# Kernel tuning notes

Hardware: AMD Instinct MI355X
Metric: run time of the kernel (lower is better)

The kernel has to match this reference:

```python
import jax, jax.numpy as jnp
import numpy as np


def _max_pairwise_dist(l, r):
    # l: [N, d], r: [M, d]
    # squared distances via Gram trick: ||l||^2 + ||r||^2 - 2 l.r  -> [N, M]
    l_sq = jnp.sum(l * l, axis=-1)  # [N]
    r_sq = jnp.sum(r * r, axis=-1)  # [M]
    cross = jnp.einsum('nd,md->nm', l, r)  # [N, M]
    sq_dists = l_sq[:, None] + r_sq[None, :] - 2.0 * cross
    sq_dists = jnp.maximum(sq_dists, 0.0)  # guard tiny negatives
    return jnp.sqrt(jnp.max(sq_dists))  # sqrt of max == max of sqrt (monotone)


def setup_inputs() -> dict:
    key = jax.random.key(0)
    k1, k2 = jax.random.split(key)
    N, M, D = 8192, 8192, 64
    return {
        'l_dfa_embeddings': jax.random.normal(k1, (N, D), dtype=jnp.float32),
        'r_dfa_embeddings': jax.random.normal(k2, (M, D), dtype=jnp.float32),
    }


def reference(l_dfa_embeddings, r_dfa_embeddings):
    # Max over all pairwise L2 distances between l and r state embeddings
    return _max_pairwise_dist(l_dfa_embeddings, r_dfa_embeddings)
```

## Files before the change

kernel.cpp:

```cpp
#include <hip/hip_runtime.h>
#include <hip/hip_bf16.h>
#include <math.h>


typedef __attribute__((ext_vector_type(8)))  short  short8;
typedef __attribute__((ext_vector_type(4)))  float  f32x4;
typedef __attribute__((ext_vector_type(16))) float  f32x16;

constexpr int D  = 64;
constexpr int NR = 8192;
constexpr int GX = 32;
constexpr int GY = 64;
constexpr int NSLOT = GX * GY;

__device__ __forceinline__ short f2bf(float f) {
    __hip_bfloat16 h = __float2bfloat16(f);
    return __builtin_bit_cast(short, h);
}


__global__ __launch_bounds__(256) void prepack_kernel(
    const float* __restrict__ L, const float* __restrict__ R,
    short* __restrict__ Apk, short* __restrict__ Bpk,
    float* __restrict__ lsq, float* __restrict__ rsq)
{
    const int t = blockIdx.x * 256 + threadIdx.x;
    const int r = t >> 3;
    const int j = t & 7;
    const int kk = j >> 1, kh = j & 1;
    const bool isL = (r < NR);
    const int rr = isL ? r : r - NR;

    const float* src = (isL ? L : R) + (size_t)rr * D + j * 8;
    short* pk = isL ? Apk : Bpk;

    f32x4 v0 = *reinterpret_cast<const f32x4*>(src + 0);
    f32x4 v1 = *reinterpret_cast<const f32x4*>(src + 4);

    float p = 0.f;
    #pragma unroll
    for (int e = 0; e < 4; ++e) { p = fmaf(v0[e], v0[e], p); p = fmaf(v1[e], v1[e], p); }

    short8 w;
    #pragma unroll
    for (int e = 0; e < 4; ++e) { w[e] = f2bf(v0[e]); w[4+e] = f2bf(v1[e]); }
    *reinterpret_cast<short8*>(
        pk + ((size_t)(rr >> 5) * 4 + kk) * 512 + (kh * 32 + (rr & 31)) * 8) = w;

    p += __shfl_xor(p, 1, 64);
    p += __shfl_xor(p, 2, 64);
    p += __shfl_xor(p, 4, 64);
    if (j == 0) (isL ? lsq : rsq)[rr] = p;
}

__global__ __launch_bounds__(256, 2) void pairdist_mfma_kernel(
    const short* __restrict__ Apk, const short* __restrict__ Bpk,
    const float* __restrict__ lsq, const float* __restrict__ rsq,
    float* __restrict__ slots)
{
    __shared__ __align__(16) short A_lds[4][4][64][8];
    __shared__ __align__(16) short B_lds[4][4][64][8];
    __shared__ __align__(16) float lsq_s[128];
    __shared__ __align__(16) float rsq_s[256];
    __shared__ float wmax_s[4];

    const int tid  = threadIdx.x;
    const int lane = tid & 63;
    const int wave = tid >> 6;
    const int yb = blockIdx.x;
    const int xc = blockIdx.y;

    {
        const short* At = Apk + (size_t)(xc * 4) * 2048;
        #pragma unroll
        for (int i = 0; i < 4; ++i)
            __builtin_amdgcn_global_load_lds(
                (const __attribute__((address_space(1))) unsigned int*)
                    (At + ((size_t)i * 4 + wave) * 512 + lane * 8),
                (__attribute__((address_space(3))) unsigned int*)
                    (&A_lds[i][wave][0][0]),
                16, 0, 0);
    }
    {
        #pragma unroll
        for (int s = 0; s < 4; ++s) {
            const int gsrc = yb * 8 + (s >> 1) * 4 + 2 + (s & 1);
            __builtin_amdgcn_global_load_lds(
                (const __attribute__((address_space(1))) unsigned int*)
                    (Bpk + ((size_t)gsrc * 4 + wave) * 512 + lane * 8),
                (__attribute__((address_space(3))) unsigned int*)
                    (&B_lds[s][wave][0][0]),
                16, 0, 0);
        }
    }

    if (tid < 128) lsq_s[tid] = lsq[xc * 128 + tid];
    rsq_s[tid] = rsq[yb * 256 + tid];

    const int wm = wave >> 1;
    const int wn = wave & 1;
    short8 bf[2][4];
    #pragma unroll
    for (int nj = 0; nj < 2; ++nj)
        #pragma unroll
        for (int kk = 0; kk < 4; ++kk)
            bf[nj][kk] = *reinterpret_cast<const short8*>(
                Bpk + ((size_t)(yb * 8 + wn * 4 + nj) * 4 + kk) * 512 + lane * 8);

    __syncthreads();

    const int col = lane & 31;
    const int h   = lane >> 5;
    float rq[4];
    #pragma unroll
    for (int nj = 0; nj < 4; ++nj) rq[nj] = rsq_s[wn * 128 + nj * 32 + col];

    f32x16 acc[2][4] = {};
    #pragma unroll
    for (int kk = 0; kk < 4; ++kk) {
        short8 a0 = *reinterpret_cast<const short8*>(&A_lds[wm*2+0][kk][lane][0]);
        short8 a1 = *reinterpret_cast<const short8*>(&A_lds[wm*2+1][kk][lane][0]);
        short8 b2 = *reinterpret_cast<const short8*>(&B_lds[wn*2+0][kk][lane][0]);
        short8 b3 = *reinterpret_cast<const short8*>(&B_lds[wn*2+1][kk][lane][0]);
        acc[0][0] = __builtin_amdgcn_mfma_f32_32x32x16_bf16(a0, bf[0][kk], acc[0][0], 0, 0, 0);
        acc[0][1] = __builtin_amdgcn_mfma_f32_32x32x16_bf16(a0, bf[1][kk], acc[0][1], 0, 0, 0);
        acc[0][2] = __builtin_amdgcn_mfma_f32_32x32x16_bf16(a0, b2,        acc[0][2], 0, 0, 0);
        acc[0][3] = __builtin_amdgcn_mfma_f32_32x32x16_bf16(a0, b3,        acc[0][3], 0, 0, 0);
        acc[1][0] = __builtin_amdgcn_mfma_f32_32x32x16_bf16(a1, bf[0][kk], acc[1][0], 0, 0, 0);
        acc[1][1] = __builtin_amdgcn_mfma_f32_32x32x16_bf16(a1, bf[1][kk], acc[1][1], 0, 0, 0);
        acc[1][2] = __builtin_amdgcn_mfma_f32_32x32x16_bf16(a1, b2,        acc[1][2], 0, 0, 0);
        acc[1][3] = __builtin_amdgcn_mfma_f32_32x32x16_bf16(a1, b3,        acc[1][3], 0, 0, 0);
    }

    float lmax = 0.f;
    #pragma unroll
    for (int mi = 0; mi < 2; ++mi) {
        const int rbase = (wm * 2 + mi) * 32 + 4 * h;
        f32x4 lq[4];
        lq[0] = *reinterpret_cast<const f32x4*>(&lsq_s[rbase +  0]);
        lq[1] = *reinterpret_cast<const f32x4*>(&lsq_s[rbase +  8]);
        lq[2] = *reinterpret_cast<const f32x4*>(&lsq_s[rbase + 16]);
        lq[3] = *reinterpret_cast<const f32x4*>(&lsq_s[rbase + 24]);
        #pragma unroll
        for (int nj = 0; nj < 4; ++nj) {
            float x[16];
            #pragma unroll
            for (int g = 0; g < 4; ++g)
                #pragma unroll
                for (int e = 0; e < 4; ++e)
                    x[g*4+e] = fmaf(-2.f, acc[mi][nj][g*4+e], lq[g][e]);
            float y0 = fmaxf(x[0],  x[1]),  y1 = fmaxf(x[2],  x[3]);
            float y2 = fmaxf(x[4],  x[5]),  y3 = fmaxf(x[6],  x[7]);
            float y4 = fmaxf(x[8],  x[9]),  y5 = fmaxf(x[10], x[11]);
            float y6 = fmaxf(x[12], x[13]), y7 = fmaxf(x[14], x[15]);
            float z0 = fmaxf(y0, y1), z1 = fmaxf(y2, y3);
            float z2 = fmaxf(y4, y5), z3 = fmaxf(y6, y7);
            float m  = fmaxf(fmaxf(z0, z1), fmaxf(z2, z3));
            lmax = fmaxf(lmax, m + rq[nj]);
        }
    }

    #pragma unroll
    for (int off = 32; off >= 1; off >>= 1)
        lmax = fmaxf(lmax, __shfl_xor(lmax, off, 64));
    if (lane == 0) wmax_s[wave] = lmax;
    __syncthreads();
    if (tid == 0) {
        float bmax = fmaxf(fmaxf(wmax_s[0], wmax_s[1]), fmaxf(wmax_s[2], wmax_s[3]));
        slots[blockIdx.y * GX + blockIdx.x] = fmaxf(bmax, 0.f);
    }
}

__global__ __launch_bounds__(512) void finalize_kernel(
    const float* __restrict__ slots, float* __restrict__ out)
{
    __shared__ float wred[8];
    const int tid = threadIdx.x;
    float v = slots[tid];
    #pragma unroll
    for (int i = 1; i < NSLOT / 512; ++i)
        v = fmaxf(v, slots[tid + i * 512]);
    #pragma unroll
    for (int off = 32; off >= 1; off >>= 1)
        v = fmaxf(v, __shfl_xor(v, off, 64));
    if ((tid & 63) == 0) wred[tid >> 6] = v;
    __syncthreads();
    if (tid == 0) {
        float m = wred[0];
        #pragma unroll
        for (int i = 1; i < 8; ++i) m = fmaxf(m, wred[i]);
        out[0] = sqrtf(m);
    }
}

extern "C" void kernel_launch(void* const* d_in, const int* in_sizes, int n_in,
                              void* d_out, int out_size, void* d_ws, size_t ws_size,
                              hipStream_t stream) {
    const float* L = (const float*)d_in[0];
    const float* R = (const float*)d_in[1];

    short* Apk = (short*)d_ws;
    short* Bpk = Apk + (size_t)NR * D;
    float* lsqg = (float*)(Bpk + (size_t)NR * D);
    float* rsqg = lsqg + NR;
    float* slots = rsqg + NR;

    prepack_kernel<<<(2 * NR * 8) / 256, 256, 0, stream>>>(L, R, Apk, Bpk, lsqg, rsqg);
    pairdist_mfma_kernel<<<dim3(GX, GY), dim3(256), 0, stream>>>(Apk, Bpk, lsqg, rsqg, slots);
    finalize_kernel<<<1, 512, 0, stream>>>(slots, (float*)d_out);
}
```

Before: 24.08 us.

## Hold A fragments in registers and stream B tiles with running max accumulator

```diff
diff --git a/kernel.cpp b/kernel.cpp
--- a/kernel.cpp
+++ b/kernel.cpp
@@ -9,9 +9,7 @@
 
 constexpr int D  = 64;
 constexpr int NR = 8192;
-constexpr int GX = 32;
-constexpr int GY = 64;
-constexpr int NSLOT = GX * GY;
+constexpr int NSLOT = 1024;
 
 __device__ __forceinline__ short f2bf(float f) {
     __hip_bfloat16 h = __float2bfloat16(f);
@@ -53,112 +51,101 @@
     if (j == 0) (isL ? lsq : rsq)[rr] = p;
 }
 
-__global__ __launch_bounds__(256, 2) void pairdist_mfma_kernel(
+__global__ __launch_bounds__(256, 3) void pairdist_mfma_kernel(
     const short* __restrict__ Apk, const short* __restrict__ Bpk,
     const float* __restrict__ lsq, const float* __restrict__ rsq,
     float* __restrict__ slots)
 {
-    __shared__ __align__(16) short A_lds[4][4][64][8];
-    __shared__ __align__(16) short B_lds[4][4][64][8];
-    __shared__ __align__(16) float lsq_s[128];
-    __shared__ __align__(16) float rsq_s[256];
+    __shared__ float lsq_s[128];
+    __shared__ __align__(16) float rsq_s[512];
     __shared__ float wmax_s[4];
 
     const int tid  = threadIdx.x;
     const int lane = tid & 63;
     const int wave = tid >> 6;
+    const int wm = wave >> 1;
+    const int wn = wave & 1;
     const int yb = blockIdx.x;
     const int xc = blockIdx.y;
 
-    {
-        const short* At = Apk + (size_t)(xc * 4) * 2048;
-        #pragma unroll
-        for (int i = 0; i < 4; ++i)
-            __builtin_amdgcn_global_load_lds(
-                (const __attribute__((address_space(1))) unsigned int*)
-                    (At + ((size_t)i * 4 + wave) * 512 + lane * 8),
-                (__attribute__((address_space(3))) unsigned int*)
-                    (&A_lds[i][wave][0][0]),
-                16, 0, 0);
-    }
-    {
-        #pragma unroll
-        for (int s = 0; s < 4; ++s) {
-            const int gsrc = yb * 8 + (s >> 1) * 4 + 2 + (s & 1);
-            __builtin_amdgcn_global_load_lds(
-                (const __attribute__((address_space(1))) unsigned int*)
-                    (Bpk + ((size_t)gsrc * 4 + wave) * 512 + lane * 8),
-                (__attribute__((address_space(3))) unsigned int*)
-                    (&B_lds[s][wave][0][0]),
-                16, 0, 0);
-        }
-    }
+    if (tid < 128) lsq_s[tid] = lsq[xc * 128 + tid];
+    rsq_s[tid]       = rsq[yb * 512 + tid];
+    rsq_s[256 + tid] = rsq[yb * 512 + 256 + tid];
 
-    if (tid < 128) lsq_s[tid] = lsq[xc * 128 + tid];
-    rsq_s[tid] = rsq[yb * 256 + tid];
-
-    const int wm = wave >> 1;
-    const int wn = wave & 1;
-    short8 bf[2][4];
+    short8 af[2][4];
     #pragma unroll
-    for (int nj = 0; nj < 2; ++nj)
+    for (int mi = 0; mi < 2; ++mi)
         #pragma unroll
         for (int kk = 0; kk < 4; ++kk)
-            bf[nj][kk] = *reinterpret_cast<const short8*>(
-                Bpk + ((size_t)(yb * 8 + wn * 4 + nj) * 4 + kk) * 512 + lane * 8);
+            af[mi][kk] = *reinterpret_cast<const short8*>(
+                Apk + ((size_t)(xc * 4 + wm * 2 + mi) * 4 + kk) * 512 + lane * 8);
 
     __syncthreads();
 
     const int col = lane & 31;
     const int h   = lane >> 5;
-    float rq[4];
+
+    f32x16 sm[2];
     #pragma unroll
-    for (int nj = 0; nj < 4; ++nj) rq[nj] = rsq_s[wn * 128 + nj * 32 + col];
+    for (int r = 0; r < 16; ++r) { sm[0][r] = -3.0e38f; sm[1][r] = -3.0e38f; }
 
-    f32x16 acc[2][4] = {};
+    short8 bf[2][4];
     #pragma unroll
-    for (int kk = 0; kk < 4; ++kk) {
-        short8 a0 = *reinterpret_cast<const short8*>(&A_lds[wm*2+0][kk][lane][0]);
-        short8 a1 = *reinterpret_cast<const short8*>(&A_lds[wm*2+1][kk][lane][0]);
-        short8 b2 = *reinterpret_cast<const short8*>(&B_lds[wn*2+0][kk][lane][0]);
-        short8 b3 = *reinterpret_cast<const short8*>(&B_lds[wn*2+1][kk][lane][0]);
-        acc[0][0] = __builtin_amdgcn_mfma_f32_32x32x16_bf16(a0, bf[0][kk], acc[0][0], 0, 0, 0);
-        acc[0][1] = __builtin_amdgcn_mfma_f32_32x32x16_bf16(a0, bf[1][kk], acc[0][1], 0, 0, 0);
-        acc[0][2] = __builtin_amdgcn_mfma_f32_32x32x16_bf16(a0, b2,        acc[0][2], 0, 0, 0);
-        acc[0][3] = __builtin_amdgcn_mfma_f32_32x32x16_bf16(a0, b3,        acc[0][3], 0, 0, 0);
-        acc[1][0] = __builtin_amdgcn_mfma_f32_32x32x16_bf16(a1, bf[0][kk], acc[1][0], 0, 0, 0);
-        acc[1][1] = __builtin_amdgcn_mfma_f32_32x32x16_bf16(a1, bf[1][kk], acc[1][1], 0, 0, 0);
-        acc[1][2] = __builtin_amdgcn_mfma_f32_32x32x16_bf16(a1, b2,        acc[1][2], 0, 0, 0);
-        acc[1][3] = __builtin_amdgcn_mfma_f32_32x32x16_bf16(a1, b3,        acc[1][3], 0, 0, 0);
+    for (int kk = 0; kk < 4; ++kk)
+        bf[0][kk] = *reinterpret_cast<const short8*>(
+            Bpk + ((size_t)(yb * 16 + wn) * 4 + kk) * 512 + lane * 8);
+
+    #pragma unroll
+    for (int t = 0; t < 8; ++t) {
+        const int cur = t & 1;
+        if (t < 7) {
+            const int cgB = yb * 16 + (t + 1) * 2 + wn;
+            #pragma unroll
+            for (int kk = 0; kk < 4; ++kk)
+                bf[cur ^ 1][kk] = *reinterpret_cast<const short8*>(
+                    Bpk + ((size_t)cgB * 4 + kk) * 512 + lane * 8);
+        }
+
+        f32x16 acc[2] = {};
+        #pragma unroll
+        for (int kk = 0; kk < 4; ++kk) {
+            acc[0] = __builtin_amdgcn_mfma_f32_32x32x16_bf16(af[0][kk], bf[cur][kk], acc[0], 0, 0, 0);
+            acc[1] = __builtin_amdgcn_mfma_f32_32x32x16_bf16(af[1][kk], bf[cur][kk], acc[1], 0, 0, 0);
+        }
+
+        const float rq = rsq_s[t * 64 + wn * 32 + col];
+        #pragma unroll
+        for (int r = 0; r < 16; ++r) {
+            sm[0][r] = fmaxf(sm[0][r], fmaf(-2.f, acc[0][r], rq));
+            sm[1][r] = fmaxf(sm[1][r], fmaf(-2.f, acc[1][r], rq));
+        }
     }
 
     float lmax = 0.f;
     #pragma unroll
     for (int mi = 0; mi < 2; ++mi) {
-        const int rbase = (wm * 2 + mi) * 32 + 4 * h;
-        f32x4 lq[4];
-        lq[0] = *reinterpret_cast<const f32x4*>(&lsq_s[rbase +  0]);
-        lq[1] = *reinterpret_cast<const f32x4*>(&lsq_s[rbase +  8]);
-        lq[2] = *reinterpret_cast<const f32x4*>(&lsq_s[rbase + 16]);
-        lq[3] = *reinterpret_cast<const f32x4*>(&lsq_s[rbase + 24]);
+        const int rbase = wm * 64 + mi * 32 + 4 * h;
+        f32x4 lq0 = *reinterpret_cast<const f32x4*>(&lsq_s[rbase +  0]);
+        f32x4 lq1 = *reinterpret_cast<const f32x4*>(&lsq_s[rbase +  8]);
+        f32x4 lq2 = *reinterpret_cast<const f32x4*>(&lsq_s[rbase + 16]);
+        f32x4 lq3 = *reinterpret_cast<const f32x4*>(&lsq_s[rbase + 24]);
+        float c[16];
         #pragma unroll
-        for (int nj = 0; nj < 4; ++nj) {
-            float x[16];
-            #pragma unroll
-            for (int g = 0; g < 4; ++g)
-                #pragma unroll
-                for (int e = 0; e < 4; ++e)
-                    x[g*4+e] = fmaf(-2.f, acc[mi][nj][g*4+e], lq[g][e]);
-            float y0 = fmaxf(x[0],  x[1]),  y1 = fmaxf(x[2],  x[3]);
-            float y2 = fmaxf(x[4],  x[5]),  y3 = fmaxf(x[6],  x[7]);
-            float y4 = fmaxf(x[8],  x[9]),  y5 = fmaxf(x[10], x[11]);
-            float y6 = fmaxf(x[12], x[13]), y7 = fmaxf(x[14], x[15]);
-            float z0 = fmaxf(y0, y1), z1 = fmaxf(y2, y3);
-            float z2 = fmaxf(y4, y5), z3 = fmaxf(y6, y7);
-            float m  = fmaxf(fmaxf(z0, z1), fmaxf(z2, z3));
-            lmax = fmaxf(lmax, m + rq[nj]);
+        for (int e = 0; e < 4; ++e) {
+            c[0  + e] = lq0[e] + sm[mi][0  + e];
+            c[4  + e] = lq1[e] + sm[mi][4  + e];
+            c[8  + e] = lq2[e] + sm[mi][8  + e];
+            c[12 + e] = lq3[e] + sm[mi][12 + e];
         }
+        float y0 = fmaxf(c[0],  c[1]),  y1 = fmaxf(c[2],  c[3]);
+        float y2 = fmaxf(c[4],  c[5]),  y3 = fmaxf(c[6],  c[7]);
+        float y4 = fmaxf(c[8],  c[9]),  y5 = fmaxf(c[10], c[11]);
+        float y6 = fmaxf(c[12], c[13]), y7 = fmaxf(c[14], c[15]);
+        float z0 = fmaxf(y0, y1), z1 = fmaxf(y2, y3);
+        float z2 = fmaxf(y4, y5), z3 = fmaxf(y6, y7);
+        lmax = fmaxf(lmax, fmaxf(fmaxf(z0, z1), fmaxf(z2, z3)));
     }
+    lmax = fmaxf(lmax, 0.f);
 
     #pragma unroll
     for (int off = 32; off >= 1; off >>= 1)
@@ -167,7 +154,7 @@
     __syncthreads();
     if (tid == 0) {
         float bmax = fmaxf(fmaxf(wmax_s[0], wmax_s[1]), fmaxf(wmax_s[2], wmax_s[3]));
-        slots[blockIdx.y * GX + blockIdx.x] = fmaxf(bmax, 0.f);
+        slots[blockIdx.y * 16 + blockIdx.x] = bmax;
     }
 }
 
@@ -176,10 +163,7 @@
 {
     __shared__ float wred[8];
     const int tid = threadIdx.x;
-    float v = slots[tid];
-    #pragma unroll
-    for (int i = 1; i < NSLOT / 512; ++i)
-        v = fmaxf(v, slots[tid + i * 512]);
+    float v = fmaxf(slots[tid], slots[tid + 512]);
     #pragma unroll
     for (int off = 32; off >= 1; off >>= 1)
         v = fmaxf(v, __shfl_xor(v, off, 64));
@@ -206,6 +190,6 @@
     float* slots = rsqg + NR;
 
     prepack_kernel<<<(2 * NR * 8) / 256, 256, 0, stream>>>(L, R, Apk, Bpk, lsqg, rsqg);
-    pairdist_mfma_kernel<<<dim3(GX, GY), dim3(256), 0, stream>>>(Apk, Bpk, lsqg, rsqg, slots);
+    pairdist_mfma_kernel<<<dim3(16, 64), dim3(256), 0, stream>>>(Apk, Bpk, lsqg, rsqg, slots);
     finalize_kernel<<<1, 512, 0, stream>>>(slots, (float*)d_out);
 }
```

Result: slower. 26.19 us (+8.8%).
